# Performance work log

Measured on AMD Instinct MI355X. Metric: run time of the kernel, lower is better.

The kernel has to match this reference:

```python
import jax, jax.numpy as jnp
import numpy as np

D_H, D_MODEL, N_HEADS = 512, 2048, 8
HEAD_DIM = D_MODEL // N_HEADS
B, T = 4, 4096


def setup_inputs() -> dict:
    key = jax.random.key(0)
    ks = jax.random.split(key, 8)
    s_dm = 1.0 / np.sqrt(D_MODEL)
    s_dh = 1.0 / np.sqrt(D_H)
    return {
        "last_hidden": jax.random.normal(ks[0], (B, T, D_MODEL), dtype=jnp.float32),
        "zH": jax.random.normal(ks[1], (B, 1, D_H), dtype=jnp.float32),
        # weights stored as (in, out): y = x @ W  (equivalent to torch Linear with W.T)
        "W_mem": jax.random.normal(ks[2], (D_H, D_MODEL), dtype=jnp.float32) * s_dh,
        "W_q": jax.random.normal(ks[3], (D_MODEL, D_MODEL), dtype=jnp.float32) * s_dm,
        "W_k": jax.random.normal(ks[4], (D_MODEL, D_MODEL), dtype=jnp.float32) * s_dm,
        "W_v": jax.random.normal(ks[5], (D_MODEL, D_MODEL), dtype=jnp.float32) * s_dm,
        "W_o": jax.random.normal(ks[6], (D_MODEL, D_MODEL), dtype=jnp.float32) * s_dm,
        "gate": jnp.asarray(0.1, dtype=jnp.float32),
    }


def reference(last_hidden, zH, W_mem, W_q, W_k, W_v, W_o, gate):
    Bb, Tt, D = last_hidden.shape
    h, hd = N_HEADS, HEAD_DIM
    mem = zH @ W_mem                                   # (B, 1, D)
    Q = (last_hidden @ W_q).reshape(Bb, Tt, h, hd)     # (B, T, h, hd)
    K = (mem @ W_k).reshape(Bb, 1, h, hd)              # (B, 1, h, hd)
    V = (mem @ W_v).reshape(Bb, 1, h, hd)
    # att_logits: (B, h, T, 1); KV length is 1 so softmax -> ones (kept faithful)
    att_logits = jnp.einsum("bthd,bshd->bhts", Q, K) / np.sqrt(hd).astype(np.float32)
    att = jax.nn.softmax(att_logits, axis=-1)
    out = jnp.einsum("bhts,bshd->bthd", att, V).reshape(Bb, Tt, D)
    out = out @ W_o
    return last_hidden + jax.nn.sigmoid(gate) * out
```

## Files before the change

kernel.cpp:

```cpp
#include <hip/hip_runtime.h>

#define D_H     512
#define D_MODEL 2048
#define B_      4
#define T_      4096

typedef float vfloat4 __attribute__((ext_vector_type(4)));
typedef float vfloat2 __attribute__((ext_vector_type(2)));

template <int KCHUNK>
__global__ __launch_bounds__(256) void gemv4_splitk_v2(
        const float* __restrict__ x,
        const float* __restrict__ W,
        float* __restrict__ out,
        int K, int N) {
    __shared__ float xs[4][KCHUNK];
    const int tid = threadIdx.x;
    const int j2  = (blockIdx.x * blockDim.x + tid) * 2;
    const int k0  = blockIdx.y * KCHUNK;

    for (int i = tid; i < 4 * KCHUNK; i += blockDim.x) {
        int b = i / KCHUNK, k = i - b * KCHUNK;
        xs[b][k] = x[b * K + k0 + k];
    }
    __syncthreads();

    vfloat2 a0 = {0.f, 0.f}, a1 = {0.f, 0.f}, a2 = {0.f, 0.f}, a3 = {0.f, 0.f};
    const float* Wp = W + (long)k0 * N + j2;
#pragma unroll 8
    for (int k = 0; k < KCHUNK; ++k) {
        vfloat2 w = *reinterpret_cast<const vfloat2*>(Wp + (long)k * N);
        float x0 = xs[0][k], x1 = xs[1][k], x2 = xs[2][k], x3 = xs[3][k];
        a0.x = fmaf(x0, w.x, a0.x);  a0.y = fmaf(x0, w.y, a0.y);
        a1.x = fmaf(x1, w.x, a1.x);  a1.y = fmaf(x1, w.y, a1.y);
        a2.x = fmaf(x2, w.x, a2.x);  a2.y = fmaf(x2, w.y, a2.y);
        a3.x = fmaf(x3, w.x, a3.x);  a3.y = fmaf(x3, w.y, a3.y);
    }
    atomicAdd(&out[0 * N + j2],     a0.x);
    atomicAdd(&out[0 * N + j2 + 1], a0.y);
    atomicAdd(&out[1 * N + j2],     a1.x);
    atomicAdd(&out[1 * N + j2 + 1], a1.y);
    atomicAdd(&out[2 * N + j2],     a2.x);
    atomicAdd(&out[2 * N + j2 + 1], a2.y);
    atomicAdd(&out[3 * N + j2],     a3.x);
    atomicAdd(&out[3 * N + j2 + 1], a3.y);
}

__global__ __launch_bounds__(256) void broadcast_add(
        const vfloat4* __restrict__ lh,
        const float* __restrict__ r,
        const float* __restrict__ gate,
        vfloat4* __restrict__ out,
        long nchunks) {
    float g = gate[0];
    float s = 1.0f / (1.0f + __expf(-g));

    const long stride = (long)gridDim.x * blockDim.x;
    for (long i = (long)blockIdx.x * blockDim.x + threadIdx.x;
         i < nchunks; i += stride) {
        long e0 = i * 4;
        int  b  = (int)(e0 >> 23);
        int  d  = (int)(e0 & (D_MODEL - 1));

        vfloat4 rv = *reinterpret_cast<const vfloat4*>(r + b * D_MODEL + d);
        vfloat4 v  = __builtin_nontemporal_load(lh + i);

        vfloat4 o;
        o.x = fmaf(s, rv.x, v.x);
        o.y = fmaf(s, rv.y, v.y);
        o.z = fmaf(s, rv.z, v.z);
        o.w = fmaf(s, rv.w, v.w);
        __builtin_nontemporal_store(o, out + i);
    }
}

extern "C" void kernel_launch(void* const* d_in, const int* in_sizes, int n_in,
                              void* d_out, int out_size, void* d_ws, size_t ws_size,
                              hipStream_t stream) {
    const float* lh    = (const float*)d_in[0];
    const float* zH    = (const float*)d_in[1];
    const float* W_mem = (const float*)d_in[2];
    const float* W_v   = (const float*)d_in[5];
    const float* W_o   = (const float*)d_in[6];
    const float* gate  = (const float*)d_in[7];
    float* out = (float*)d_out;

    float* mem = (float*)d_ws;
    float* V   = mem + B_ * D_MODEL;
    float* r   = V   + B_ * D_MODEL;
    (void)hipMemsetAsync(d_ws, 0, (size_t)3 * B_ * D_MODEL * sizeof(float), stream);

    dim3 blk(256);

    {
        dim3 grd(D_MODEL / (256 * 2), D_H / 16);
        gemv4_splitk_v2<16><<<grd, blk, 0, stream>>>(zH, W_mem, mem, D_H, D_MODEL);
    }
    {
        dim3 grd(D_MODEL / (256 * 2), D_MODEL / 32);
        gemv4_splitk_v2<32><<<grd, blk, 0, stream>>>(mem, W_v, V, D_MODEL, D_MODEL);
    }
    {
        dim3 grd(D_MODEL / (256 * 2), D_MODEL / 32);
        gemv4_splitk_v2<32><<<grd, blk, 0, stream>>>(V, W_o, r, D_MODEL, D_MODEL);
    }
    {
        long nchunks = (long)B_ * T_ * D_MODEL / 4;
        dim3 grd(2048);
        broadcast_add<<<grd, blk, 0, stream>>>(
            (const vfloat4*)lh, r, gate, (vfloat4*)out, nchunks);
    }
}
```

Before: 286.6 us.

## Fuse GEMV chain and broadcast add into one cooperative grid-synced kernel

Replaces the memset, three split-K GEMV launches and the broadcast-add launch with a single cooperative kernel of 512 blocks. Grid-wide syncs separate the workspace zeroing, the GEMV stages and the streaming residual add. The goal is to remove per-launch overhead and the inter-kernel gaps. The GEMV inner loop now computes one column per thread instead of two, and the non-cooperative fallback path is regridded to match. In exchange, the bandwidth-bound streaming phase runs on a smaller fixed grid, and the grid barriers add their own cost.

```diff
diff --git a/kernel.cpp b/kernel.cpp
--- a/kernel.cpp
+++ b/kernel.cpp
@@ -1,4 +1,7 @@
 #include <hip/hip_runtime.h>
+#include <hip/hip_cooperative_groups.h>
+
+namespace cg = cooperative_groups;
 
 #define D_H     512
 #define D_MODEL 2048
@@ -9,62 +12,101 @@
 typedef float vfloat2 __attribute__((ext_vector_type(2)));
 
 template <int KCHUNK>
-__global__ __launch_bounds__(256) void gemv4_splitk_v2(
-        const float* __restrict__ x,
-        const float* __restrict__ W,
-        float* __restrict__ out,
-        int K, int N) {
+__device__ __forceinline__ void gemv_slice(
+        const float* __restrict__ x, const float* __restrict__ W,
+        float* __restrict__ out, int K, int N, int jb, int kb, int tid) {
     __shared__ float xs[4][KCHUNK];
-    const int tid = threadIdx.x;
-    const int j2  = (blockIdx.x * blockDim.x + tid) * 2;
-    const int k0  = blockIdx.y * KCHUNK;
-
-    for (int i = tid; i < 4 * KCHUNK; i += blockDim.x) {
+    const int j  = jb * 256 + tid;
+    const int k0 = kb * KCHUNK;
+    for (int i = tid; i < 4 * KCHUNK; i += 256) {
         int b = i / KCHUNK, k = i - b * KCHUNK;
         xs[b][k] = x[b * K + k0 + k];
     }
     __syncthreads();
-
-    vfloat2 a0 = {0.f, 0.f}, a1 = {0.f, 0.f}, a2 = {0.f, 0.f}, a3 = {0.f, 0.f};
-    const float* Wp = W + (long)k0 * N + j2;
+    float a0 = 0.f, a1 = 0.f, a2 = 0.f, a3 = 0.f;
+    const float* Wp = W + (long)k0 * N + j;
 #pragma unroll 8
     for (int k = 0; k < KCHUNK; ++k) {
-        vfloat2 w = *reinterpret_cast<const vfloat2*>(Wp + (long)k * N);
-        float x0 = xs[0][k], x1 = xs[1][k], x2 = xs[2][k], x3 = xs[3][k];
-        a0.x = fmaf(x0, w.x, a0.x);  a0.y = fmaf(x0, w.y, a0.y);
-        a1.x = fmaf(x1, w.x, a1.x);  a1.y = fmaf(x1, w.y, a1.y);
-        a2.x = fmaf(x2, w.x, a2.x);  a2.y = fmaf(x2, w.y, a2.y);
-        a3.x = fmaf(x3, w.x, a3.x);  a3.y = fmaf(x3, w.y, a3.y);
+        float w = Wp[(long)k * N];
+        a0 = fmaf(xs[0][k], w, a0);
+        a1 = fmaf(xs[1][k], w, a1);
+        a2 = fmaf(xs[2][k], w, a2);
+        a3 = fmaf(xs[3][k], w, a3);
     }
-    atomicAdd(&out[0 * N + j2],     a0.x);
-    atomicAdd(&out[0 * N + j2 + 1], a0.y);
-    atomicAdd(&out[1 * N + j2],     a1.x);
-    atomicAdd(&out[1 * N + j2 + 1], a1.y);
-    atomicAdd(&out[2 * N + j2],     a2.x);
-    atomicAdd(&out[2 * N + j2 + 1], a2.y);
-    atomicAdd(&out[3 * N + j2],     a3.x);
-    atomicAdd(&out[3 * N + j2 + 1], a3.y);
+    atomicAdd(&out[0 * N + j], a0);
+    atomicAdd(&out[1 * N + j], a1);
+    atomicAdd(&out[2 * N + j], a2);
+    atomicAdd(&out[3 * N + j], a3);
+}
+
+__global__ __launch_bounds__(256) void fused_bridge(
+        const float* __restrict__ lh, const float* __restrict__ zH,
+        const float* __restrict__ W_mem, const float* __restrict__ W_v,
+        const float* __restrict__ W_o, const float* __restrict__ gate,
+        float* __restrict__ out, float* __restrict__ ws) {
+    const int tid  = threadIdx.x;
+    const int bid  = blockIdx.x;
+    const int gtid = bid * 256 + tid;
+    float* mem = ws;
+    float* V   = ws + B_ * D_MODEL;
+    float* r   = ws + 2 * B_ * D_MODEL;
+    cg::grid_group grid = cg::this_grid();
+
+    if (gtid < 3 * B_ * D_MODEL) ws[gtid] = 0.f;
+    grid.sync();
+
+    if (bid < 256) gemv_slice<16>(zH, W_mem, mem, D_H, D_MODEL, bid & 7, bid >> 3, tid);
+    grid.sync();
+
+    gemv_slice<32>(mem, W_v, V, D_MODEL, D_MODEL, bid & 7, bid >> 3, tid);
+    grid.sync();
+
+    gemv_slice<32>(V, W_o, r, D_MODEL, D_MODEL, bid & 7, bid >> 3, tid);
+    grid.sync();
+
+    const float g = gate[0];
+    const float s = 1.0f / (1.0f + __expf(-g));
+    const vfloat4* lh4 = reinterpret_cast<const vfloat4*>(lh);
+    vfloat4* out4 = reinterpret_cast<vfloat4*>(out);
+#pragma unroll 4
+    for (int it = 0; it < 64; ++it) {
+        long i  = (long)gtid + (long)it * (512 * 256);
+        long e0 = i * 4;
+        int  b  = (int)(e0 >> 23);
+        int  d  = (int)(e0 & (D_MODEL - 1));
+        vfloat4 rv = *reinterpret_cast<const vfloat4*>(r + b * D_MODEL + d);
+        vfloat4 v  = __builtin_nontemporal_load(lh4 + i);
+        vfloat4 o;
+        o.x = fmaf(s, rv.x, v.x);
+        o.y = fmaf(s, rv.y, v.y);
+        o.z = fmaf(s, rv.z, v.z);
+        o.w = fmaf(s, rv.w, v.w);
+        __builtin_nontemporal_store(o, out4 + i);
+    }
+}
+
+template <int KCHUNK>
+__global__ __launch_bounds__(256) void gemv4_splitk(
+        const float* __restrict__ x, const float* __restrict__ W,
+        float* __restrict__ out, int K, int N) {
+    gemv_slice<KCHUNK>(x, W, out, K, N, (int)blockIdx.x, (int)blockIdx.y,
+                       (int)threadIdx.x);
 }
 
 __global__ __launch_bounds__(256) void broadcast_add(
-        const vfloat4* __restrict__ lh,
-        const float* __restrict__ r,
-        const float* __restrict__ gate,
-        vfloat4* __restrict__ out,
+        const vfloat4* __restrict__ lh, const float* __restrict__ r,
+        const float* __restrict__ gate, vfloat4* __restrict__ out,
         long nchunks) {
     float g = gate[0];
     float s = 1.0f / (1.0f + __expf(-g));
-
     const long stride = (long)gridDim.x * blockDim.x;
     for (long i = (long)blockIdx.x * blockDim.x + threadIdx.x;
          i < nchunks; i += stride) {
         long e0 = i * 4;
         int  b  = (int)(e0 >> 23);
         int  d  = (int)(e0 & (D_MODEL - 1));
-
         vfloat4 rv = *reinterpret_cast<const vfloat4*>(r + b * D_MODEL + d);
         vfloat4 v  = __builtin_nontemporal_load(lh + i);
-
         vfloat4 o;
         o.x = fmaf(s, rv.x, v.x);
         o.y = fmaf(s, rv.y, v.y);
@@ -84,25 +126,35 @@
     const float* W_o   = (const float*)d_in[6];
     const float* gate  = (const float*)d_in[7];
     float* out = (float*)d_out;
+    float* ws  = (float*)d_ws;
 
-    float* mem = (float*)d_ws;
+    {
+        void* args[] = {(void*)&lh, (void*)&zH, (void*)&W_mem, (void*)&W_v,
+                        (void*)&W_o, (void*)&gate, (void*)&out, (void*)&ws};
+        hipError_t e = hipLaunchCooperativeKernel((const void*)fused_bridge,
+                                                  dim3(512), dim3(256),
+                                                  args, 0, stream);
+        if (e == hipSuccess) return;
+        (void)hipGetLastError();
+    }
+
+    float* mem = ws;
     float* V   = mem + B_ * D_MODEL;
     float* r   = V   + B_ * D_MODEL;
     (void)hipMemsetAsync(d_ws, 0, (size_t)3 * B_ * D_MODEL * sizeof(float), stream);
 
     dim3 blk(256);
-
     {
-        dim3 grd(D_MODEL / (256 * 2), D_H / 16);
-        gemv4_splitk_v2<16><<<grd, blk, 0, stream>>>(zH, W_mem, mem, D_H, D_MODEL);
+        dim3 grd(D_MODEL / 256, 32);
+        gemv4_splitk<16><<<grd, blk, 0, stream>>>(zH, W_mem, mem, D_H, D_MODEL);
     }
     {
-        dim3 grd(D_MODEL / (256 * 2), D_MODEL / 32);
-        gemv4_splitk_v2<32><<<grd, blk, 0, stream>>>(mem, W_v, V, D_MODEL, D_MODEL);
+        dim3 grd(D_MODEL / 256, 64);
+        gemv4_splitk<32><<<grd, blk, 0, stream>>>(mem, W_v, V, D_MODEL, D_MODEL);
     }
     {
-        dim3 grd(D_MODEL / (256 * 2), D_MODEL / 32);
-        gemv4_splitk_v2<32><<<grd, blk, 0, stream>>>(V, W_o, r, D_MODEL, D_MODEL);
+        dim3 grd(D_MODEL / 256, 64);
+        gemv4_splitk<32><<<grd, blk, 0, stream>>>(V, W_o, r, D_MODEL, D_MODEL);
     }
     {
         long nchunks = (long)B_ * T_ * D_MODEL / 4;
```

New measurement: 495.7 us. 1.73x slower.
